# Kernel tuning notes

Hardware: AMD Instinct MI355X
Metric: run time of the kernel (lower is better)

The kernel has to match this reference:

```python
import jax, jax.numpy as jnp
import numpy as np

N, NFEAT = 8192, 128

def _unif(k, shape, fan_out):
    s = 1.0 / np.sqrt(fan_out)
    return jax.random.uniform(k, shape, jnp.float32, -s, s)

def setup_inputs() -> dict:
    key = jax.random.key(0)
    ks = jax.random.split(key, 10)
    x = jax.random.normal(ks[0], (N, NFEAT), jnp.float32)
    adj = jax.random.uniform(ks[1], (N, N), jnp.float32)  # all > 0 -> full degree
    W1 = _unif(ks[2], (NFEAT, 10), 10); b1 = _unif(ks[3], (10,), 10)
    W2 = _unif(ks[4], (10, 5), 5);      b2 = _unif(ks[5], (5,), 5)
    fc1_W = _unif(ks[6], (5, 5), 5);    fc1_b = _unif(ks[7], (5,), 5)
    fc_W = _unif(ks[8], (5, 2), 2);     fc_b = _unif(ks[9], (2,), 2)
    return dict(x=x, adj=adj, W1=W1, b1=b1, W2=W2, b2=b2,
                fc1_W=fc1_W, fc1_b=fc1_b, fc_W=fc_W, fc_b=fc_b)

def _gcn(x, adj, W, b):
    # D = diag(row-wise count of adj > 0); A_tilda = D^-1/2 (A + I) D^-1/2
    deg = jnp.sum((adj > 0.0).astype(x.dtype), axis=1)
    dinv = deg ** -0.5                       # [N]
    s = (x @ W) * dinv[:, None]              # D^-1/2 @ (X W), [N, out]
    out = dinv[:, None] * (adj @ s + s)      # D^-1/2 @ (A + I) @ s
    return out + b

def reference(x, adj, W1, b1, W2, b2, fc1_W, fc1_b, fc_W, fc_b):
    h = jax.nn.relu(_gcn(x, adj, W1, b1))    # [N, 10]
    h = _gcn(h, adj, W2, b2)                 # [N, 5]
    z = jax.nn.relu(jnp.mean(h, axis=0))     # [5]
    z2 = jax.nn.relu(z @ fc1_W + fc1_b)      # [5]
    y = jax.nn.sigmoid(z2 @ fc_W + fc_b)     # [2]
    return (z, y)
```

## Files before the change

kernel.cpp:

```cpp
#include <hip/hip_runtime.h>
#include <math.h>

#define NN 8192
#define NF 128


__global__ __launch_bounds__(256) void kA(const float* __restrict__ adj,
                                          float* __restrict__ dinv,
                                          float* __restrict__ c0,
                                          int* __restrict__ Zcount,
                                          int* __restrict__ Zlist) {
    const int t = threadIdx.x;
    const int lane = t & 63, wid = t >> 6;
    const int rowBase = blockIdx.x * 32;
    float4 csum[8];
#pragma unroll
    for (int q = 0; q < 8; q++) csum[q] = make_float4(0.f, 0.f, 0.f, 0.f);
    __shared__ int wsum[4];

    for (int r = 0; r < 32; r++) {
        const int i = rowBase + r;
        const float4* arow = (const float4*)(adj + (size_t)i * NN);
        int cnt = 0;
#pragma unroll
        for (int it = 0; it < 8; it++) {
            float4 a = arow[it * 256 + t];
            csum[it].x += a.x; csum[it].y += a.y;
            csum[it].z += a.z; csum[it].w += a.w;
            cnt += (a.x > 0.f) + (a.y > 0.f) + (a.z > 0.f) + (a.w > 0.f);
        }
#pragma unroll
        for (int off = 32; off > 0; off >>= 1) cnt += __shfl_xor(cnt, off, 64);
        if (lane == 0) wsum[wid] = cnt;
        __syncthreads();
        if (t == 0) {
            int d = wsum[0] + wsum[1] + wsum[2] + wsum[3];
            dinv[i] = rsqrtf((float)d);
            if (d != NN) { int p = atomicAdd(Zcount, 1); Zlist[p] = i; }
        }
        __syncthreads();
    }
#pragma unroll
    for (int it = 0; it < 8; it++) {
        int j = (it * 256 + t) * 4;
        atomicAdd(&c0[j + 0], csum[it].x);
        atomicAdd(&c0[j + 1], csum[it].y);
        atomicAdd(&c0[j + 2], csum[it].z);
        atomicAdd(&c0[j + 3], csum[it].w);
    }
}

__global__ __launch_bounds__(256) void kC(const float* __restrict__ adj,
                                          const float* __restrict__ dinv,
                                          float* __restrict__ c0,
                                          const int* __restrict__ Zcount,
                                          const int* __restrict__ Zlist) {
    int j = blockIdx.x * 256 + threadIdx.x;
    const float dinv0 = rsqrtf((float)NN);
    float v = c0[j] * dinv0;
    int zc = *Zcount;
    for (int p = 0; p < zc; p++) {
        int zi = Zlist[p];
        v += (dinv[zi] - dinv0) * adj[(size_t)zi * NN + j];
    }
    c0[j] = v;
}

__global__ __launch_bounds__(256) void kS1(const float* __restrict__ x,
                                           const float* __restrict__ W1,
                                           const float* __restrict__ dinv,
                                           float* __restrict__ s1) {
    __shared__ float sW[NF * 10];
    for (int i = threadIdx.x; i < NF * 10; i += 256) sW[i] = W1[i];
    __syncthreads();
    int tid = blockIdx.x * 256 + threadIdx.x;
    int j = tid / 10, k = tid % 10;
    const float4* xr = (const float4*)(x + (size_t)j * NF);
    float s = 0.f;
#pragma unroll
    for (int f4 = 0; f4 < 32; f4++) {
        float4 a = xr[f4];
        s += a.x * sW[(f4 * 4 + 0) * 10 + k] + a.y * sW[(f4 * 4 + 1) * 10 + k]
           + a.z * sW[(f4 * 4 + 2) * 10 + k] + a.w * sW[(f4 * 4 + 3) * 10 + k];
    }
    s1[tid] = s * dinv[j];
}

__global__ __launch_bounds__(256) void kP(const float* __restrict__ adj,
                                          const float* __restrict__ s1,
                                          const float* __restrict__ dinv,
                                          const float* __restrict__ b1,
                                          float* __restrict__ h) {
    const int t = threadIdx.x;
    const int lane = t & 63, wid = t >> 6;
    const int i0 = blockIdx.x * 16 + wid * 4;
    float acc[4][10];
#pragma unroll
    for (int r = 0; r < 4; r++)
#pragma unroll
        for (int k = 0; k < 10; k++) acc[r][k] = 0.f;

    const float4* a0p = (const float4*)(adj + (size_t)(i0 + 0) * NN);
    const float4* a1p = (const float4*)(adj + (size_t)(i0 + 1) * NN);
    const float4* a2p = (const float4*)(adj + (size_t)(i0 + 2) * NN);
    const float4* a3p = (const float4*)(adj + (size_t)(i0 + 3) * NN);

    for (int it = 0; it < 32; it++) {
        int vi = it * 64 + lane;
        float4 a0 = a0p[vi], a1 = a1p[vi], a2 = a2p[vi], a3 = a3p[vi];
        const float4* sp = (const float4*)(s1 + (size_t)vi * 40);
        float sv[40];
#pragma unroll
        for (int q = 0; q < 10; q++) {
            float4 v = sp[q];
            sv[q * 4 + 0] = v.x; sv[q * 4 + 1] = v.y;
            sv[q * 4 + 2] = v.z; sv[q * 4 + 3] = v.w;
        }
#pragma unroll
        for (int k = 0; k < 10; k++) {
            acc[0][k] += a0.x * sv[k] + a0.y * sv[10 + k] + a0.z * sv[20 + k] + a0.w * sv[30 + k];
            acc[1][k] += a1.x * sv[k] + a1.y * sv[10 + k] + a1.z * sv[20 + k] + a1.w * sv[30 + k];
            acc[2][k] += a2.x * sv[k] + a2.y * sv[10 + k] + a2.z * sv[20 + k] + a2.w * sv[30 + k];
            acc[3][k] += a3.x * sv[k] + a3.y * sv[10 + k] + a3.z * sv[20 + k] + a3.w * sv[30 + k];
        }
    }
#pragma unroll
    for (int r = 0; r < 4; r++)
#pragma unroll
        for (int k = 0; k < 10; k++)
#pragma unroll
            for (int off = 32; off > 0; off >>= 1)
                acc[r][k] += __shfl_xor(acc[r][k], off, 64);

    if (lane == 0) {
#pragma unroll
        for (int r = 0; r < 4; r++) {
            int i = i0 + r;
            float di = dinv[i];
#pragma unroll
            for (int k = 0; k < 10; k++) {
                float v = di * (acc[r][k] + s1[i * 10 + k]) + b1[k];
                h[i * 10 + k] = fmaxf(v, 0.f);
            }
        }
    }
}

__global__ __launch_bounds__(256) void kF1(const float* __restrict__ h,
                                           const float* __restrict__ dinv,
                                           const float* __restrict__ c0,
                                           const float* __restrict__ W2,
                                           float* __restrict__ accum) {
    int j = blockIdx.x * 256 + threadIdx.x;
    float hv[10];
#pragma unroll
    for (int m = 0; m < 10; m++) hv[m] = h[j * 10 + m];
    float dj = dinv[j], cj = c0[j];
    float p[10];
#pragma unroll
    for (int k = 0; k < 5; k++) {
        float s = 0.f;
#pragma unroll
        for (int m = 0; m < 10; m++) s += hv[m] * W2[m * 5 + k];
        s *= dj;
        p[k] = cj * s;
        p[5 + k] = dj * s;
    }
#pragma unroll
    for (int q = 0; q < 10; q++) {
        float v = p[q];
#pragma unroll
        for (int off = 32; off > 0; off >>= 1) v += __shfl_xor(v, off, 64);
        if ((threadIdx.x & 63) == 0) atomicAdd(&accum[q], v);
    }
}

__global__ void kF2(const float* __restrict__ accum, const float* __restrict__ b2,
                    const float* __restrict__ fc1W, const float* __restrict__ fc1b,
                    const float* __restrict__ fcW, const float* __restrict__ fcb,
                    float* __restrict__ out) {
    if (threadIdx.x == 0 && blockIdx.x == 0) {
        float z[5];
        for (int k = 0; k < 5; k++) {
            float v = (accum[k] + accum[5 + k]) * (1.f / (float)NN) + b2[k];
            z[k] = fmaxf(v, 0.f);
            out[k] = z[k];
        }
        float z2[5];
        for (int m = 0; m < 5; m++) {
            float v = fc1b[m];
            for (int k = 0; k < 5; k++) v += z[k] * fc1W[k * 5 + m];
            z2[m] = fmaxf(v, 0.f);
        }
        for (int n = 0; n < 2; n++) {
            float v = fcb[n];
            for (int m = 0; m < 5; m++) v += z2[m] * fcW[m * 2 + n];
            out[5 + n] = 1.f / (1.f + expf(-v));
        }
    }
}

extern "C" void kernel_launch(void* const* d_in, const int* in_sizes, int n_in,
                              void* d_out, int out_size, void* d_ws, size_t ws_size,
                              hipStream_t stream) {
    const float* x    = (const float*)d_in[0];
    const float* adj  = (const float*)d_in[1];
    const float* W1   = (const float*)d_in[2];
    const float* b1   = (const float*)d_in[3];
    const float* W2   = (const float*)d_in[4];
    const float* b2   = (const float*)d_in[5];
    const float* fc1W = (const float*)d_in[6];
    const float* fc1b = (const float*)d_in[7];
    const float* fcW  = (const float*)d_in[8];
    const float* fcb  = (const float*)d_in[9];
    (void)in_sizes; (void)n_in; (void)out_size; (void)ws_size;

    float* ws    = (float*)d_ws;
    float* dinv  = ws;
    float* c0    = ws + 8192;
    float* s1    = ws + 16384;
    float* h     = ws + 98304;
    float* accum = ws + 180224;
    int*   Zcount = (int*)(ws + 180240);
    int*   Zlist  = (int*)(ws + 180244);
    float* out = (float*)d_out;

    hipMemsetAsync(c0, 0, 8192 * sizeof(float), stream);
    hipMemsetAsync(accum, 0, 20 * sizeof(float), stream);

    kA <<<256, 256, 0, stream>>>(adj, dinv, c0, Zcount, Zlist);
    kC <<<32,  256, 0, stream>>>(adj, dinv, c0, Zcount, Zlist);
    kS1<<<320, 256, 0, stream>>>(x, W1, dinv, s1);
    kP <<<512, 256, 0, stream>>>(adj, s1, dinv, b1, h);
    kF1<<<32,  256, 0, stream>>>(h, dinv, c0, W2, accum);
    kF2<<<1,   64,  0, stream>>>(accum, b2, fc1W, fc1b, fcW, fcb, out);
}
```

Baseline: 517.0 us.

## Fuse degree, column-sum and first aggregation into a single adjacency pass

The degree-count and column-sum kernel is merged with the first A@s aggregation so the 8192x8192 adjacency is streamed once instead of twice. To make this possible, the aggregation is computed against unscaled XW under the assumption of uniform degree, then corrected by a new kernel that adds terms only for rows recorded in the non-full-degree list. Column sums are written to per-block slabs and reduced in a separate kernel, which removes the float atomics. This costs an extra 16 MB slab write and read, and the correction work grows with the number of non-full-degree rows.

```diff
diff --git a/kernel.cpp b/kernel.cpp
--- a/kernel.cpp
+++ b/kernel.cpp
@@ -5,71 +5,9 @@
 #define NF 128
 
 
-__global__ __launch_bounds__(256) void kA(const float* __restrict__ adj,
-                                          float* __restrict__ dinv,
-                                          float* __restrict__ c0,
-                                          int* __restrict__ Zcount,
-                                          int* __restrict__ Zlist) {
-    const int t = threadIdx.x;
-    const int lane = t & 63, wid = t >> 6;
-    const int rowBase = blockIdx.x * 32;
-    float4 csum[8];
-#pragma unroll
-    for (int q = 0; q < 8; q++) csum[q] = make_float4(0.f, 0.f, 0.f, 0.f);
-    __shared__ int wsum[4];
-
-    for (int r = 0; r < 32; r++) {
-        const int i = rowBase + r;
-        const float4* arow = (const float4*)(adj + (size_t)i * NN);
-        int cnt = 0;
-#pragma unroll
-        for (int it = 0; it < 8; it++) {
-            float4 a = arow[it * 256 + t];
-            csum[it].x += a.x; csum[it].y += a.y;
-            csum[it].z += a.z; csum[it].w += a.w;
-            cnt += (a.x > 0.f) + (a.y > 0.f) + (a.z > 0.f) + (a.w > 0.f);
-        }
-#pragma unroll
-        for (int off = 32; off > 0; off >>= 1) cnt += __shfl_xor(cnt, off, 64);
-        if (lane == 0) wsum[wid] = cnt;
-        __syncthreads();
-        if (t == 0) {
-            int d = wsum[0] + wsum[1] + wsum[2] + wsum[3];
-            dinv[i] = rsqrtf((float)d);
-            if (d != NN) { int p = atomicAdd(Zcount, 1); Zlist[p] = i; }
-        }
-        __syncthreads();
-    }
-#pragma unroll
-    for (int it = 0; it < 8; it++) {
-        int j = (it * 256 + t) * 4;
-        atomicAdd(&c0[j + 0], csum[it].x);
-        atomicAdd(&c0[j + 1], csum[it].y);
-        atomicAdd(&c0[j + 2], csum[it].z);
-        atomicAdd(&c0[j + 3], csum[it].w);
-    }
-}
-
-__global__ __launch_bounds__(256) void kC(const float* __restrict__ adj,
-                                          const float* __restrict__ dinv,
-                                          float* __restrict__ c0,
-                                          const int* __restrict__ Zcount,
-                                          const int* __restrict__ Zlist) {
-    int j = blockIdx.x * 256 + threadIdx.x;
-    const float dinv0 = rsqrtf((float)NN);
-    float v = c0[j] * dinv0;
-    int zc = *Zcount;
-    for (int p = 0; p < zc; p++) {
-        int zi = Zlist[p];
-        v += (dinv[zi] - dinv0) * adj[(size_t)zi * NN + j];
-    }
-    c0[j] = v;
-}
-
-__global__ __launch_bounds__(256) void kS1(const float* __restrict__ x,
+__global__ __launch_bounds__(256) void kS0(const float* __restrict__ x,
                                            const float* __restrict__ W1,
-                                           const float* __restrict__ dinv,
-                                           float* __restrict__ s1) {
+                                           float* __restrict__ xw) {
     __shared__ float sW[NF * 10];
     for (int i = threadIdx.x; i < NF * 10; i += 256) sW[i] = W1[i];
     __syncthreads();
@@ -83,66 +21,147 @@
         s += a.x * sW[(f4 * 4 + 0) * 10 + k] + a.y * sW[(f4 * 4 + 1) * 10 + k]
            + a.z * sW[(f4 * 4 + 2) * 10 + k] + a.w * sW[(f4 * 4 + 3) * 10 + k];
     }
-    s1[tid] = s * dinv[j];
-}
-
-__global__ __launch_bounds__(256) void kP(const float* __restrict__ adj,
-                                          const float* __restrict__ s1,
-                                          const float* __restrict__ dinv,
-                                          const float* __restrict__ b1,
-                                          float* __restrict__ h) {
+    xw[tid] = s;
+}
+
+__global__ __launch_bounds__(256) void kMain(const float* __restrict__ adj,
+                                             const float* __restrict__ xw,
+                                             float* __restrict__ dinv,
+                                             float* __restrict__ yraw,
+                                             float* __restrict__ slab,
+                                             int* __restrict__ Zcount,
+                                             int* __restrict__ Zlist) {
     const int t = threadIdx.x;
     const int lane = t & 63, wid = t >> 6;
-    const int i0 = blockIdx.x * 16 + wid * 4;
-    float acc[4][10];
-#pragma unroll
-    for (int r = 0; r < 4; r++)
-#pragma unroll
-        for (int k = 0; k < 10; k++) acc[r][k] = 0.f;
-
-    const float4* a0p = (const float4*)(adj + (size_t)(i0 + 0) * NN);
-    const float4* a1p = (const float4*)(adj + (size_t)(i0 + 1) * NN);
-    const float4* a2p = (const float4*)(adj + (size_t)(i0 + 2) * NN);
-    const float4* a3p = (const float4*)(adj + (size_t)(i0 + 3) * NN);
-
-    for (int it = 0; it < 32; it++) {
-        int vi = it * 64 + lane;
-        float4 a0 = a0p[vi], a1 = a1p[vi], a2 = a2p[vi], a3 = a3p[vi];
-        const float4* sp = (const float4*)(s1 + (size_t)vi * 40);
-        float sv[40];
-#pragma unroll
-        for (int q = 0; q < 10; q++) {
-            float4 v = sp[q];
-            sv[q * 4 + 0] = v.x; sv[q * 4 + 1] = v.y;
-            sv[q * 4 + 2] = v.z; sv[q * 4 + 3] = v.w;
-        }
-#pragma unroll
-        for (int k = 0; k < 10; k++) {
-            acc[0][k] += a0.x * sv[k] + a0.y * sv[10 + k] + a0.z * sv[20 + k] + a0.w * sv[30 + k];
-            acc[1][k] += a1.x * sv[k] + a1.y * sv[10 + k] + a1.z * sv[20 + k] + a1.w * sv[30 + k];
-            acc[2][k] += a2.x * sv[k] + a2.y * sv[10 + k] + a2.z * sv[20 + k] + a2.w * sv[30 + k];
-            acc[3][k] += a3.x * sv[k] + a3.y * sv[10 + k] + a3.z * sv[20 + k] + a3.w * sv[30 + k];
-        }
-    }
-#pragma unroll
-    for (int r = 0; r < 4; r++)
-#pragma unroll
-        for (int k = 0; k < 10; k++)
+    const int rowBase = blockIdx.x * 16;
+    float* myslab = slab + (size_t)blockIdx.x * NN;
+    __shared__ float sh[4][44];
+
+    float4 csum[8];
+#pragma unroll
+    for (int q = 0; q < 8; q++) csum[q] = make_float4(0.f, 0.f, 0.f, 0.f);
+
+    for (int tile = 0; tile < 4; tile++) {
+        const int i0 = rowBase + tile * 4;
+        const float4* r0 = (const float4*)(adj + (size_t)(i0 + 0) * NN);
+        const float4* r1 = (const float4*)(adj + (size_t)(i0 + 1) * NN);
+        const float4* r2 = (const float4*)(adj + (size_t)(i0 + 2) * NN);
+        const float4* r3 = (const float4*)(adj + (size_t)(i0 + 3) * NN);
+        float acc[4][10];
+        int cnt[4] = {0, 0, 0, 0};
+#pragma unroll
+        for (int r = 0; r < 4; r++)
+#pragma unroll
+            for (int k = 0; k < 10; k++) acc[r][k] = 0.f;
+
+#pragma unroll
+        for (int it = 0; it < 8; it++) {
+            const int c4 = it * 256 + t;
+            float4 a0 = r0[c4], a1 = r1[c4], a2 = r2[c4], a3 = r3[c4];
+            const float4* xp = (const float4*)(xw + (size_t)c4 * 40);
+            float sv[40];
+#pragma unroll
+            for (int q = 0; q < 10; q++) {
+                float4 v = xp[q];
+                sv[q * 4 + 0] = v.x; sv[q * 4 + 1] = v.y;
+                sv[q * 4 + 2] = v.z; sv[q * 4 + 3] = v.w;
+            }
+#pragma unroll
+            for (int k = 0; k < 10; k++) {
+                acc[0][k] += a0.x * sv[k] + a0.y * sv[10 + k] + a0.z * sv[20 + k] + a0.w * sv[30 + k];
+                acc[1][k] += a1.x * sv[k] + a1.y * sv[10 + k] + a1.z * sv[20 + k] + a1.w * sv[30 + k];
+                acc[2][k] += a2.x * sv[k] + a2.y * sv[10 + k] + a2.z * sv[20 + k] + a2.w * sv[30 + k];
+                acc[3][k] += a3.x * sv[k] + a3.y * sv[10 + k] + a3.z * sv[20 + k] + a3.w * sv[30 + k];
+            }
+            csum[it].x += a0.x + a1.x + a2.x + a3.x;
+            csum[it].y += a0.y + a1.y + a2.y + a3.y;
+            csum[it].z += a0.z + a1.z + a2.z + a3.z;
+            csum[it].w += a0.w + a1.w + a2.w + a3.w;
+            cnt[0] += (a0.x > 0.f) + (a0.y > 0.f) + (a0.z > 0.f) + (a0.w > 0.f);
+            cnt[1] += (a1.x > 0.f) + (a1.y > 0.f) + (a1.z > 0.f) + (a1.w > 0.f);
+            cnt[2] += (a2.x > 0.f) + (a2.y > 0.f) + (a2.z > 0.f) + (a2.w > 0.f);
+            cnt[3] += (a3.x > 0.f) + (a3.y > 0.f) + (a3.z > 0.f) + (a3.w > 0.f);
+        }
+#pragma unroll
+        for (int r = 0; r < 4; r++) {
+#pragma unroll
+            for (int k = 0; k < 10; k++)
+#pragma unroll
+                for (int off = 32; off > 0; off >>= 1)
+                    acc[r][k] += __shfl_xor(acc[r][k], off, 64);
 #pragma unroll
             for (int off = 32; off > 0; off >>= 1)
-                acc[r][k] += __shfl_xor(acc[r][k], off, 64);
-
-    if (lane == 0) {
-#pragma unroll
-        for (int r = 0; r < 4; r++) {
-            int i = i0 + r;
-            float di = dinv[i];
-#pragma unroll
-            for (int k = 0; k < 10; k++) {
-                float v = di * (acc[r][k] + s1[i * 10 + k]) + b1[k];
-                h[i * 10 + k] = fmaxf(v, 0.f);
+                cnt[r] += __shfl_xor(cnt[r], off, 64);
+        }
+        if (lane == 0) {
+#pragma unroll
+            for (int q = 0; q < 40; q++) sh[wid][q] = acc[q / 10][q % 10];
+#pragma unroll
+            for (int r = 0; r < 4; r++) sh[wid][40 + r] = (float)cnt[r];
+        }
+        __syncthreads();
+        if (t < 44) {
+            float v = sh[0][t] + sh[1][t] + sh[2][t] + sh[3][t];
+            if (t < 40) {
+                yraw[(i0 + t / 10) * 10 + (t % 10)] = v;
+            } else {
+                int r = t - 40;
+                int d = (int)v;
+                dinv[i0 + r] = rsqrtf((float)d);
+                if (d != NN) { int p = atomicAdd(Zcount, 1); Zlist[p] = i0 + r; }
             }
         }
+        __syncthreads();
+    }
+#pragma unroll
+    for (int it = 0; it < 8; it++)
+        ((float4*)myslab)[it * 256 + t] = csum[it];
+}
+
+__global__ __launch_bounds__(256) void kRedC(const float* __restrict__ adj,
+                                             const float* __restrict__ dinv,
+                                             const float* __restrict__ slab,
+                                             float* __restrict__ c0,
+                                             const int* __restrict__ Zcount,
+                                             const int* __restrict__ Zlist) {
+    int j = blockIdx.x * 256 + threadIdx.x;
+    float s = 0.f;
+    for (int b = 0; b < 512; b++) s += slab[(size_t)b * NN + j];
+    const float dinv0 = rsqrtf((float)NN);
+    float v = s * dinv0;
+    int zc = *Zcount;
+    for (int p = 0; p < zc; p++) {
+        int zi = Zlist[p];
+        v += (dinv[zi] - dinv0) * adj[(size_t)zi * NN + j];
+    }
+    c0[j] = v;
+}
+
+__global__ __launch_bounds__(128) void kFix(const float* __restrict__ adj,
+                                            const float* __restrict__ xw,
+                                            const float* __restrict__ yraw,
+                                            const float* __restrict__ dinv,
+                                            const float* __restrict__ b1,
+                                            float* __restrict__ h,
+                                            const int* __restrict__ Zcount,
+                                            const int* __restrict__ Zlist) {
+    int i = blockIdx.x * 128 + threadIdx.x;
+    const float dinv0 = rsqrtf((float)NN);
+    float corr[10];
+#pragma unroll
+    for (int k = 0; k < 10; k++) corr[k] = 0.f;
+    int zc = *Zcount;
+    for (int p = 0; p < zc; p++) {
+        int zj = Zlist[p];
+        float w = (dinv[zj] - dinv0) * adj[(size_t)i * NN + zj];
+#pragma unroll
+        for (int k = 0; k < 10; k++) corr[k] += w * xw[zj * 10 + k];
+    }
+    float di = dinv[i];
+#pragma unroll
+    for (int k = 0; k < 10; k++) {
+        float v = di * (dinv0 * yraw[i * 10 + k] + corr[k] + di * xw[i * 10 + k]) + b1[k];
+        h[i * 10 + k] = fmaxf(v, 0.f);
     }
 }
 
@@ -215,23 +234,24 @@
     const float* fcb  = (const float*)d_in[9];
     (void)in_sizes; (void)n_in; (void)out_size; (void)ws_size;
 
-    float* ws    = (float*)d_ws;
-    float* dinv  = ws;
-    float* c0    = ws + 8192;
-    float* s1    = ws + 16384;
-    float* h     = ws + 98304;
-    float* accum = ws + 180224;
-    int*   Zcount = (int*)(ws + 180240);
-    int*   Zlist  = (int*)(ws + 180244);
-    float* out = (float*)d_out;
-
-    hipMemsetAsync(c0, 0, 8192 * sizeof(float), stream);
-    hipMemsetAsync(accum, 0, 20 * sizeof(float), stream);
-
-    kA <<<256, 256, 0, stream>>>(adj, dinv, c0, Zcount, Zlist);
-    kC <<<32,  256, 0, stream>>>(adj, dinv, c0, Zcount, Zlist);
-    kS1<<<320, 256, 0, stream>>>(x, W1, dinv, s1);
-    kP <<<512, 256, 0, stream>>>(adj, s1, dinv, b1, h);
-    kF1<<<32,  256, 0, stream>>>(h, dinv, c0, W2, accum);
-    kF2<<<1,   64,  0, stream>>>(accum, b2, fc1W, fc1b, fcW, fcb, out);
-}
+    float* ws     = (float*)d_ws;
+    float* dinv   = ws;
+    float* c0     = ws + 8192;
+    float* xw     = ws + 16384;
+    float* yraw   = ws + 98304;
+    float* h      = ws + 180224;
+    float* accum  = ws + 262144;
+    int*   Zcount = (int*)(ws + 262154);
+    int*   Zlist  = (int*)(ws + 262155);
+    float* slab   = ws + 270592;
+    float* out    = (float*)d_out;
+
+    hipMemsetAsync(accum, 0, 48, stream);
+
+    kS0  <<<320, 256, 0, stream>>>(x, W1, xw);
+    kMain<<<512, 256, 0, stream>>>(adj, xw, dinv, yraw, slab, Zcount, Zlist);
+    kRedC<<<32,  256, 0, stream>>>(adj, dinv, slab, c0, Zcount, Zlist);
+    kFix <<<64,  128, 0, stream>>>(adj, xw, yraw, dinv, b1, h, Zcount, Zlist);
+    kF1  <<<32,  256, 0, stream>>>(h, dinv, c0, W2, accum);
+    kF2  <<<1,   64,  0, stream>>>(accum, b2, fc1W, fc1b, fcW, fcb, out);
+}
```

Result: slower. 635.3 us (+22.9%).
